# Kernel optimization log

Measured on AMD Instinct MI355X. Metric: run time of the kernel, lower is better.

Reference implementation:

```python
import jax, jax.numpy as jnp
import numpy as np

WS = (2, 6, 12)          # window_size (Z, H, W)
DIM = 192
HEADS = 6
TOW = 240                # type_of_windows = (8//2)*(360//6)
NW = 720                 # total number of windows = 3 * TOW
L = WS[0] * WS[1] * WS[2]  # 144 tokens per window


def _position_index(ws):
    """Replicates EarthAttention3D._construct_index (static int index)."""
    zi = np.arange(ws[0]); zj = -np.arange(ws[0]) * ws[0]
    hi = np.arange(ws[1]); hj = -np.arange(ws[1]) * ws[1]
    w = np.arange(ws[2])
    c1 = np.stack(np.meshgrid(zi, hi, w, indexing='ij')).reshape(3, -1)
    c2 = np.stack(np.meshgrid(zj, hj, w, indexing='ij')).reshape(3, -1)
    coords = (c1[:, :, None] - c2[:, None, :]).transpose(1, 2, 0)  # (L, L, 3)
    coords[:, :, 2] += ws[2] - 1
    coords[:, :, 1] *= 2 * ws[2] - 1
    coords[:, :, 0] *= (2 * ws[2] - 1) * ws[1] * ws[1]
    return coords.sum(-1).reshape(-1)  # (L*L,)

POS_INDEX = jnp.asarray(_position_index(WS))


def setup_inputs() -> dict:
    key = jax.random.key(0)
    ks = jax.random.split(key, 4)
    table_len = (2 * WS[2] - 1) * WS[1] * WS[1] * WS[0] * WS[0]  # 3312
    return {
        "x": jax.random.normal(ks[0], (NW, L, DIM), jnp.float32),
        "mask": jnp.zeros((NW, L, L), jnp.float32),
        "w1": jax.random.normal(ks[1], (3 * DIM, DIM), jnp.float32) * 0.02,
        "b1": jnp.zeros((3 * DIM,), jnp.float32),
        "w2": jax.random.normal(ks[2], (DIM, DIM), jnp.float32) * 0.02,
        "b2": jnp.zeros((DIM,), jnp.float32),
        "bias_table": jax.random.normal(ks[3], (table_len, TOW, HEADS), jnp.float32) * 0.02,
    }


def reference(x, mask, w1, b1, w2, b2, bias_table):
    Wn, Ltok, dim = x.shape
    hd = dim // HEADS
    scale = hd ** -0.5
    # qkv projection: (Wn, L, 3, H, hd) -> q,k,v each (Wn, H, L, hd)
    qkv = (x @ w1.T + b1).reshape(Wn, Ltok, 3, HEADS, hd)
    qkv = jnp.transpose(qkv, (2, 0, 3, 1, 4))
    q, k, v = qkv[0], qkv[1], qkv[2]
    attn = jnp.einsum('whid,whjd->whij', q * scale, k)  # (Wn, H, L, L)
    # Earth-specific bias: gather table -> (L, L, TOW, H) -> (TOW, H, L, L)
    bias = bias_table[POS_INDEX].reshape(Ltok, Ltok, TOW, HEADS)
    bias = jnp.transpose(bias, (2, 3, 0, 1))
    # tile across window axis exactly like the concat loop, then slice
    reps = Wn // TOW + 1
    bias = jnp.tile(bias, (reps, 1, 1, 1))[:Wn][None]  # (1, Wn, H, L, L)
    attn = attn[None] + bias                            # (1, Wn, H, L, L)
    attn = attn + mask[None, :, None, :, :]             # mask.unsqueeze(1).unsqueeze(0)
    attn = jax.nn.softmax(attn, axis=-1)
    out = jnp.einsum('bwhij,whjd->bwhid', attn, v)      # (1, Wn, H, L, hd)
    out = jnp.transpose(out, (0, 1, 3, 2, 4)).reshape(Wn, Ltok, dim)
    out = out @ w2.T + b2
    return out
```

## Files before the change

kernel.cpp:

```cpp
#include <hip/hip_runtime.h>
#include <cstdint>
#include <cstddef>


using short8 = __attribute__((ext_vector_type(8))) short;
using f32x4  = __attribute__((ext_vector_type(4))) float;

constexpr int kNW = 720;
constexpr float kScale = 0.17677669529663687f;
constexpr size_t kQKVElems = (size_t)kNW * 6 * 144 * 32;

__device__ __forceinline__ ushort bf16_rne(float f) {
  uint u = __builtin_bit_cast(uint, f);
  return (ushort)((u + 0x7FFFu + ((u >> 16) & 1u)) >> 16);
}
__device__ __forceinline__ float bf16_to_f(ushort h) {
  uint u = ((uint)h) << 16;
  return __builtin_bit_cast(float, u);
}
__device__ __forceinline__ uint pack_hl(float f) {
  const ushort h = bf16_rne(f);
  const ushort l = bf16_rne(f - bf16_to_f(h));
  return ((uint)h << 16) | l;
}

__global__ __launch_bounds__(256) void prep_kernel(
    const float* __restrict__ src, ushort* __restrict__ dh,
    ushort* __restrict__ dl, int n)
{
  const int i = blockIdx.x * 256 + threadIdx.x;
  if (i < n) {
    const float f = src[i];
    const ushort h = bf16_rne(f);
    dh[i] = h;
    dl[i] = bf16_rne(f - bf16_to_f(h));
  }
}

__global__ __launch_bounds__(256) void btT_kernel(
    const float* __restrict__ bt, float* __restrict__ btT)
{
  __shared__ float T[48][49];
  const int pb = (blockIdx.x % 69) * 48;
  const int bb = (blockIdx.x / 69) * 48;
  const int tid = threadIdx.x;
  for (int f = tid; f < 2304; f += 256) {
    const int r = f / 48, c = f % 48;
    T[r][c] = bt[(size_t)(pb + r) * 1440 + bb + c];
  }
  __syncthreads();
  for (int f = tid; f < 2304; f += 256) {
    const int r = f % 48, c = f / 48;
    btT[(size_t)(bb + c) * 3312 + pb + r] = T[r][c];
  }
}

template <bool IS_QKV>
__global__ __launch_bounds__(512) void gemm_kernel(
    const float* __restrict__ Xf, const uint* __restrict__ Xp,
    const ushort* __restrict__ Wh, const ushort* __restrict__ Wl,
    const float* __restrict__ bias,
    uint* __restrict__ qp, uint* __restrict__ kp, uint* __restrict__ vp,
    float* __restrict__ fout)
{
  __shared__ ushort Ah[128][40], Al[128][40];
  __shared__ ushort Bh[192][40], Bl[192][40];

  const int bid = blockIdx.x;
  const int mtile = IS_QKV ? bid / 3 : bid;
  const int col0  = IS_QKV ? (bid % 3) * 192 : 0;
  const int row0 = mtile * 128;
  const int tid = threadIdx.x;
  const int wave = tid >> 6, lane = tid & 63;
  const int rr = lane & 15, kg = lane >> 4;
  const int wm = wave >> 2, wn = wave & 3;

  f32x4 acc[4][3];
#pragma unroll
  for (int a = 0; a < 4; ++a)
#pragma unroll
    for (int b = 0; b < 3; ++b) acc[a][b] = (f32x4){0.f, 0.f, 0.f, 0.f};

  for (int kc = 0; kc < 192; kc += 32) {
#pragma unroll
    for (int u = 0; u < 2; ++u) {
      const int sl = tid + u * 512;
      const int r = sl >> 3, s = sl & 7;
      if constexpr (IS_QKV) {
        float4 xv = *(const float4*)&Xf[(size_t)(row0 + r) * 192 + kc + s * 4];
        ushort4 hv, lv;
        hv.x = bf16_rne(xv.x); lv.x = bf16_rne(xv.x - bf16_to_f(hv.x));
        hv.y = bf16_rne(xv.y); lv.y = bf16_rne(xv.y - bf16_to_f(hv.y));
        hv.z = bf16_rne(xv.z); lv.z = bf16_rne(xv.z - bf16_to_f(hv.z));
        hv.w = bf16_rne(xv.w); lv.w = bf16_rne(xv.w - bf16_to_f(hv.w));
        *(ushort4*)&Ah[r][s * 4] = hv;
        *(ushort4*)&Al[r][s * 4] = lv;
      } else {
        uint4 a = *(const uint4*)&Xp[(size_t)(row0 + r) * 192 + kc + s * 4];
        uint2 hh, ll;
        hh.x = (a.x >> 16) | (a.y & 0xffff0000u);
        hh.y = (a.z >> 16) | (a.w & 0xffff0000u);
        ll.x = (a.x & 0xffffu) | (a.y << 16);
        ll.y = (a.z & 0xffffu) | (a.w << 16);
        *(uint2*)&Ah[r][s * 4] = hh;
        *(uint2*)&Al[r][s * 4] = ll;
      }
    }
#pragma unroll
    for (int u = 0; u < 3; ++u) {
      const int idx = tid + u * 512;
      const int n = idx >> 3, s2 = idx & 7;
      const size_t g = (size_t)(col0 + n) * 192 + kc + s2 * 4;
      *(uint2*)&Bh[n][s2 * 4] = *(const uint2*)&Wh[g];
      *(uint2*)&Bl[n][s2 * 4] = *(const uint2*)&Wl[g];
    }
    __syncthreads();

    short8 ah[4], al_[4], bh[3], bl[3];
#pragma unroll
    for (int mt = 0; mt < 4; ++mt) {
      const int r = wm * 64 + mt * 16 + rr;
      ah[mt]  = *(const short8*)&Ah[r][kg * 8];
      al_[mt] = *(const short8*)&Al[r][kg * 8];
    }
#pragma unroll
    for (int nt = 0; nt < 3; ++nt) {
      const int n = wn * 48 + nt * 16 + rr;
      bh[nt] = *(const short8*)&Bh[n][kg * 8];
      bl[nt] = *(const short8*)&Bl[n][kg * 8];
    }
#pragma unroll
    for (int mt = 0; mt < 4; ++mt)
#pragma unroll
      for (int nt = 0; nt < 3; ++nt) {
        acc[mt][nt] = __builtin_amdgcn_mfma_f32_16x16x32_bf16(ah[mt],  bh[nt], acc[mt][nt], 0, 0, 0);
        acc[mt][nt] = __builtin_amdgcn_mfma_f32_16x16x32_bf16(ah[mt],  bl[nt], acc[mt][nt], 0, 0, 0);
        acc[mt][nt] = __builtin_amdgcn_mfma_f32_16x16x32_bf16(al_[mt], bh[nt], acc[mt][nt], 0, 0, 0);
      }
    __syncthreads();
  }

  if (IS_QKV) {
    const int t = col0 / 192;
    uint* dst = (t == 0) ? qp : (t == 1) ? kp : vp;
    const float sc = (t == 0) ? kScale : 1.0f;
#pragma unroll
    for (int nt = 0; nt < 3; ++nt) {
      const int c0 = wn * 48 + nt * 16;
      const int hh = c0 >> 5;
      const int d0 = (c0 & 31) + rr;
      const float bcol = bias[col0 + c0 + rr];
#pragma unroll
      for (int mt = 0; mt < 4; ++mt)
#pragma unroll
        for (int reg = 0; reg < 4; ++reg) {
          const int grow = row0 + wm * 64 + mt * 16 + kg * 4 + reg;
          const int w = grow / 144;
          const int l = grow % 144;
          dst[(((size_t)(w * 6 + hh)) * 144 + l) * 32 + d0] =
              pack_hl((acc[mt][nt][reg] + bcol) * sc);
        }
    }
  } else {
#pragma unroll
    for (int nt = 0; nt < 3; ++nt) {
      const int c = wn * 48 + nt * 16 + rr;
      const float bcol = bias[c];
#pragma unroll
      for (int mt = 0; mt < 4; ++mt)
#pragma unroll
        for (int reg = 0; reg < 4; ++reg) {
          const int grow = row0 + wm * 64 + mt * 16 + kg * 4 + reg;
          fout[(size_t)grow * 192 + c] = acc[mt][nt][reg] + bcol;
        }
    }
  }
}

__global__ __launch_bounds__(576) void attn_kernel(
    const uint* __restrict__ qp, const uint* __restrict__ kp,
    const uint* __restrict__ vp, const float* __restrict__ mask,
    const float* __restrict__ btT, uint* __restrict__ aop)
{
  __shared__ ushort Ks_[2][144][40];
  __shared__ ushort Vt[2][32][168];

  const int bid = blockIdx.x;
  const int wid = (bid & 7) * 540 + (bid >> 3);
  const int w = wid / 6, h = wid % 6;
  const int tid = threadIdx.x;
  const int wave = tid >> 6, lane = tid & 63;
  const int rr = lane & 15, kg = lane >> 4;
  const size_t base = (size_t)(w * 6 + h) * 4608;
  const float* mrow = mask + (size_t)w * 20736;
  const float* brow = btT + (size_t)((w % 240) * 6 + h) * 3312;

  const int i0 = wave * 16;
  const int i = i0 + rr;
  const int pi = 828 * (i / 72) + 23 * ((i / 12) % 6) + (i % 12) + 11;

  const uint4 qa = *(const uint4*)&qp[base + (size_t)i * 32 + kg * 8];
  const uint4 qb = *(const uint4*)&qp[base + (size_t)i * 32 + kg * 8 + 4];
  float4 mv[9], bv[9];
#pragma unroll
  for (int jt = 0; jt < 9; ++jt) {
    const int jb = jt * 16 + kg * 4;
    mv[jt] = *(const float4*)&mrow[(size_t)i * 144 + jb];
    const int pjb = 1656 * (jb / 72) + 138 * ((jb / 12) % 6) - (jb % 12);
    bv[jt] = *(const float4*)&brow[pi + pjb - 3];
  }

  for (int f = tid; f < 1152; f += 576) {
    const int l = f >> 3, d0 = (f & 7) * 4;
    const uint4 kv = *(const uint4*)&kp[base + l * 32 + d0];
    ushort4 hk, lk;
    hk.x = (ushort)(kv.x >> 16); lk.x = (ushort)(kv.x & 0xffff);
    hk.y = (ushort)(kv.y >> 16); lk.y = (ushort)(kv.y & 0xffff);
    hk.z = (ushort)(kv.z >> 16); lk.z = (ushort)(kv.z & 0xffff);
    hk.w = (ushort)(kv.w >> 16); lk.w = (ushort)(kv.w & 0xffff);
    *(ushort4*)&Ks_[0][l][d0] = hk;
    *(ushort4*)&Ks_[1][l][d0] = lk;
    const uint4 vv = *(const uint4*)&vp[base + l * 32 + d0];
    Vt[0][d0 + 0][l] = (ushort)(vv.x >> 16); Vt[1][d0 + 0][l] = (ushort)(vv.x & 0xffff);
    Vt[0][d0 + 1][l] = (ushort)(vv.y >> 16); Vt[1][d0 + 1][l] = (ushort)(vv.y & 0xffff);
    Vt[0][d0 + 2][l] = (ushort)(vv.z >> 16); Vt[1][d0 + 2][l] = (ushort)(vv.z & 0xffff);
    Vt[0][d0 + 3][l] = (ushort)(vv.w >> 16); Vt[1][d0 + 3][l] = (ushort)(vv.w & 0xffff);
  }
  if (tid < 512) {
    const int d = tid >> 4, j = 144 + (tid & 15);
    Vt[0][d][j] = 0;
    Vt[1][d][j] = 0;
  }
  __syncthreads();

  union { short8 v; uint u[4]; } QH, QL;
  QH.u[0] = (qa.x >> 16) | (qa.y & 0xffff0000u);
  QH.u[1] = (qa.z >> 16) | (qa.w & 0xffff0000u);
  QH.u[2] = (qb.x >> 16) | (qb.y & 0xffff0000u);
  QH.u[3] = (qb.z >> 16) | (qb.w & 0xffff0000u);
  QL.u[0] = (qa.x & 0xffffu) | (qa.y << 16);
  QL.u[1] = (qa.z & 0xffffu) | (qa.w << 16);
  QL.u[2] = (qb.x & 0xffffu) | (qb.y << 16);
  QL.u[3] = (qb.z & 0xffffu) | (qb.w << 16);

  f32x4 acc[9];
#pragma unroll
  for (int jt = 0; jt < 9; ++jt) {
    const short8 kah = *(const short8*)&Ks_[0][jt * 16 + rr][kg * 8];
    const short8 kal = *(const short8*)&Ks_[1][jt * 16 + rr][kg * 8];
    f32x4 c = (f32x4){0.f, 0.f, 0.f, 0.f};
    c = __builtin_amdgcn_mfma_f32_16x16x32_bf16(kah, QH.v, c, 0, 0, 0);
    c = __builtin_amdgcn_mfma_f32_16x16x32_bf16(kah, QL.v, c, 0, 0, 0);
    c = __builtin_amdgcn_mfma_f32_16x16x32_bf16(kal, QH.v, c, 0, 0, 0);
    c[0] += bv[jt].w + mv[jt].x;
    c[1] += bv[jt].z + mv[jt].y;
    c[2] += bv[jt].y + mv[jt].z;
    c[3] += bv[jt].x + mv[jt].w;
    acc[jt] = c;
  }

  float m = -1e30f;
#pragma unroll
  for (int jt = 0; jt < 9; ++jt)
    m = fmaxf(m, fmaxf(fmaxf(acc[jt][0], acc[jt][1]),
                       fmaxf(acc[jt][2], acc[jt][3])));
  m = fmaxf(m, __shfl_xor(m, 16));
  m = fmaxf(m, __shfl_xor(m, 32));
  float s = 0.f;
#pragma unroll
  for (int jt = 0; jt < 9; ++jt)
#pragma unroll
    for (int r = 0; r < 4; ++r) {
      acc[jt][r] = __expf(acc[jt][r] - m);
      s += acc[jt][r];
    }
  s += __shfl_xor(s, 16);
  s += __shfl_xor(s, 32);
  const float inv = 1.0f / s;

  uint wh_[10][2], wl_[10][2];
#pragma unroll
  for (int jt = 0; jt < 9; ++jt)
#pragma unroll
    for (int u = 0; u < 2; ++u) {
      const float p0 = acc[jt][2 * u] * inv, p1 = acc[jt][2 * u + 1] * inv;
      const ushort h0 = bf16_rne(p0), h1 = bf16_rne(p1);
      const ushort l0 = bf16_rne(p0 - bf16_to_f(h0));
      const ushort l1 = bf16_rne(p1 - bf16_to_f(h1));
      wh_[jt][u] = (uint)h0 | ((uint)h1 << 16);
      wl_[jt][u] = (uint)l0 | ((uint)l1 << 16);
    }
  wh_[9][0] = 0; wh_[9][1] = 0; wl_[9][0] = 0; wl_[9][1] = 0;

  __syncthreads();

  uint* scrw = (uint*)((ushort*)&Ks_[0][0][0] + wave * 1280);
  f32x4 oacc[2] = {(f32x4){0.f, 0.f, 0.f, 0.f}, (f32x4){0.f, 0.f, 0.f, 0.f}};
#pragma unroll
  for (int ks = 0; ks < 5; ++ks) {
    const int jtA = 2 * ks, jtB = 2 * ks + 1;
    *(uint2*)&scrw[rr * 20 + 2 * kg]           = make_uint2(wh_[jtA][0], wh_[jtA][1]);
    *(uint2*)&scrw[rr * 20 + 8 + 2 * kg]       = make_uint2(wh_[jtB][0], wh_[jtB][1]);
    *(uint2*)&scrw[320 + rr * 20 + 2 * kg]     = make_uint2(wl_[jtA][0], wl_[jtA][1]);
    *(uint2*)&scrw[320 + rr * 20 + 8 + 2 * kg] = make_uint2(wl_[jtB][0], wl_[jtB][1]);
    asm volatile("s_waitcnt lgkmcnt(0)" ::: "memory");
    const ushort* scr = (const ushort*)scrw;
    const short8 pfh = *(const short8*)&scr[rr * 40 + kg * 8];
    const short8 pfl = *(const short8*)&scr[640 + rr * 40 + kg * 8];
#pragma unroll
    for (int dt = 0; dt < 2; ++dt) {
      const short8 vfh = *(const short8*)&Vt[0][dt * 16 + rr][ks * 32 + kg * 8];
      const short8 vfl = *(const short8*)&Vt[1][dt * 16 + rr][ks * 32 + kg * 8];
      oacc[dt] = __builtin_amdgcn_mfma_f32_16x16x32_bf16(pfh, vfh, oacc[dt], 0, 0, 0);
      oacc[dt] = __builtin_amdgcn_mfma_f32_16x16x32_bf16(pfh, vfl, oacc[dt], 0, 0, 0);
      oacc[dt] = __builtin_amdgcn_mfma_f32_16x16x32_bf16(pfl, vfh, oacc[dt], 0, 0, 0);
    }
  }

#pragma unroll
  for (int dt = 0; dt < 2; ++dt)
#pragma unroll
    for (int r = 0; r < 4; ++r)
      aop[(size_t)(w * 144 + i0 + kg * 4 + r) * 192 + h * 32 + dt * 16 + rr] =
          pack_hl(oacc[dt][r]);
}

extern "C" void kernel_launch(void* const* d_in, const int* in_sizes, int n_in,
                              void* d_out, int out_size, void* d_ws, size_t ws_size,
                              hipStream_t stream)
{
  const float* x    = (const float*)d_in[0];
  const float* mask = (const float*)d_in[1];
  const float* w1   = (const float*)d_in[2];
  const float* b1   = (const float*)d_in[3];
  const float* w2   = (const float*)d_in[4];
  const float* b2   = (const float*)d_in[5];
  const float* bt   = (const float*)d_in[6];
  float* out = (float*)d_out;

  uint* qp  = (uint*)d_ws;
  uint* kp  = qp + kQKVElems;
  uint* vp  = kp + kQKVElems;
  uint* aop = vp + kQKVElems;
  ushort* w1h = (ushort*)aop;
  ushort* w1l = w1h + 110592;
  ushort* w2h = (ushort*)qp;
  ushort* w2l = w2h + 36864;
  float* btT = out;

  btT_kernel<<<69 * 30, 256, 0, stream>>>(bt, btT);
  prep_kernel<<<432, 256, 0, stream>>>(w1, w1h, w1l, 110592);
  gemm_kernel<true><<<810 * 3, 512, 0, stream>>>(
      x, nullptr, w1h, w1l, b1, qp, kp, vp, nullptr);
  attn_kernel<<<4320, 576, 0, stream>>>(qp, kp, vp, mask, btT, aop);
  prep_kernel<<<144, 256, 0, stream>>>(w2, w2h, w2l, 36864);
  gemm_kernel<false><<<810, 512, 0, stream>>>(
      nullptr, aop, w2h, w2l, b2, nullptr, nullptr, nullptr, out);
}
```

Before: 370.3 us.

## Cut attention register pressure: in-loop bias loads, lazy bf16 split, deferred normalization

```diff
diff --git a/kernel.cpp b/kernel.cpp
--- a/kernel.cpp
+++ b/kernel.cpp
@@ -22,6 +22,13 @@
   const ushort h = bf16_rne(f);
   const ushort l = bf16_rne(f - bf16_to_f(h));
   return ((uint)h << 16) | l;
+}
+__device__ __forceinline__ void split2(float a, float b, uint& hw, uint& lw) {
+  const ushort ha = bf16_rne(a), hb = bf16_rne(b);
+  const ushort la = bf16_rne(a - bf16_to_f(ha));
+  const ushort lb = bf16_rne(b - bf16_to_f(hb));
+  hw = (uint)ha | ((uint)hb << 16);
+  lw = (uint)la | ((uint)lb << 16);
 }
 
 __global__ __launch_bounds__(256) void prep_kernel(
@@ -184,6 +191,7 @@
 {
   __shared__ ushort Ks_[2][144][40];
   __shared__ ushort Vt[2][32][168];
+  __shared__ float Sinv[148];
 
   const int bid = blockIdx.x;
   const int wid = (bid & 7) * 540 + (bid >> 3);
@@ -201,14 +209,6 @@
 
   const uint4 qa = *(const uint4*)&qp[base + (size_t)i * 32 + kg * 8];
   const uint4 qb = *(const uint4*)&qp[base + (size_t)i * 32 + kg * 8 + 4];
-  float4 mv[9], bv[9];
-#pragma unroll
-  for (int jt = 0; jt < 9; ++jt) {
-    const int jb = jt * 16 + kg * 4;
-    mv[jt] = *(const float4*)&mrow[(size_t)i * 144 + jb];
-    const int pjb = 1656 * (jb / 72) + 138 * ((jb / 12) % 6) - (jb % 12);
-    bv[jt] = *(const float4*)&brow[pi + pjb - 3];
-  }
 
   for (int f = tid; f < 1152; f += 576) {
     const int l = f >> 3, d0 = (f & 7) * 4;
@@ -246,17 +246,22 @@
   f32x4 acc[9];
 #pragma unroll
   for (int jt = 0; jt < 9; ++jt) {
+    const int jb = jt * 16 + kg * 4;
+    const float4 mv = *(const float4*)&mrow[(size_t)i * 144 + jb];
+    const int pjb = 1656 * (jb / 72) + 138 * ((jb / 12) % 6) - (jb % 12);
+    const float4 bv = *(const float4*)&brow[pi + pjb - 3];
     const short8 kah = *(const short8*)&Ks_[0][jt * 16 + rr][kg * 8];
     const short8 kal = *(const short8*)&Ks_[1][jt * 16 + rr][kg * 8];
     f32x4 c = (f32x4){0.f, 0.f, 0.f, 0.f};
     c = __builtin_amdgcn_mfma_f32_16x16x32_bf16(kah, QH.v, c, 0, 0, 0);
     c = __builtin_amdgcn_mfma_f32_16x16x32_bf16(kah, QL.v, c, 0, 0, 0);
     c = __builtin_amdgcn_mfma_f32_16x16x32_bf16(kal, QH.v, c, 0, 0, 0);
-    c[0] += bv[jt].w + mv[jt].x;
-    c[1] += bv[jt].z + mv[jt].y;
-    c[2] += bv[jt].y + mv[jt].z;
-    c[3] += bv[jt].x + mv[jt].w;
+    c[0] += bv.w + mv.x;
+    c[1] += bv.z + mv.y;
+    c[2] += bv.y + mv.z;
+    c[3] += bv.x + mv.w;
     acc[jt] = c;
+    __builtin_amdgcn_sched_barrier(0x38F);
   }
 
   float m = -1e30f;
@@ -276,21 +281,7 @@
     }
   s += __shfl_xor(s, 16);
   s += __shfl_xor(s, 32);
-  const float inv = 1.0f / s;
-
-  uint wh_[10][2], wl_[10][2];
-#pragma unroll
-  for (int jt = 0; jt < 9; ++jt)
-#pragma unroll
-    for (int u = 0; u < 2; ++u) {
-      const float p0 = acc[jt][2 * u] * inv, p1 = acc[jt][2 * u + 1] * inv;
-      const ushort h0 = bf16_rne(p0), h1 = bf16_rne(p1);
-      const ushort l0 = bf16_rne(p0 - bf16_to_f(h0));
-      const ushort l1 = bf16_rne(p1 - bf16_to_f(h1));
-      wh_[jt][u] = (uint)h0 | ((uint)h1 << 16);
-      wl_[jt][u] = (uint)l0 | ((uint)l1 << 16);
-    }
-  wh_[9][0] = 0; wh_[9][1] = 0; wl_[9][0] = 0; wl_[9][1] = 0;
+  if (kg == 0) Sinv[i] = 1.0f / s;
 
   __syncthreads();
 
@@ -298,11 +289,19 @@
   f32x4 oacc[2] = {(f32x4){0.f, 0.f, 0.f, 0.f}, (f32x4){0.f, 0.f, 0.f, 0.f}};
 #pragma unroll
   for (int ks = 0; ks < 5; ++ks) {
-    const int jtA = 2 * ks, jtB = 2 * ks + 1;
-    *(uint2*)&scrw[rr * 20 + 2 * kg]           = make_uint2(wh_[jtA][0], wh_[jtA][1]);
-    *(uint2*)&scrw[rr * 20 + 8 + 2 * kg]       = make_uint2(wh_[jtB][0], wh_[jtB][1]);
-    *(uint2*)&scrw[320 + rr * 20 + 2 * kg]     = make_uint2(wl_[jtA][0], wl_[jtA][1]);
-    *(uint2*)&scrw[320 + rr * 20 + 8 + 2 * kg] = make_uint2(wl_[jtB][0], wl_[jtB][1]);
+    uint h0, h1, h2, h3, l0, l1, l2, l3;
+    split2(acc[2 * ks][0], acc[2 * ks][1], h0, l0);
+    split2(acc[2 * ks][2], acc[2 * ks][3], h1, l1);
+    if (2 * ks + 1 < 9) {
+      split2(acc[2 * ks + 1][0], acc[2 * ks + 1][1], h2, l2);
+      split2(acc[2 * ks + 1][2], acc[2 * ks + 1][3], h3, l3);
+    } else {
+      h2 = h3 = l2 = l3 = 0;
+    }
+    *(uint2*)&scrw[rr * 20 + 2 * kg]           = make_uint2(h0, h1);
+    *(uint2*)&scrw[rr * 20 + 8 + 2 * kg]       = make_uint2(h2, h3);
+    *(uint2*)&scrw[320 + rr * 20 + 2 * kg]     = make_uint2(l0, l1);
+    *(uint2*)&scrw[320 + rr * 20 + 8 + 2 * kg] = make_uint2(l2, l3);
     asm volatile("s_waitcnt lgkmcnt(0)" ::: "memory");
     const ushort* scr = (const ushort*)scrw;
     const short8 pfh = *(const short8*)&scr[rr * 40 + kg * 8];
@@ -317,12 +316,14 @@
     }
   }
 
+  const float4 sv4 = *(const float4*)&Sinv[i0 + kg * 4];
+  const float svr[4] = {sv4.x, sv4.y, sv4.z, sv4.w};
 #pragma unroll
   for (int dt = 0; dt < 2; ++dt)
 #pragma unroll
     for (int r = 0; r < 4; ++r)
       aop[(size_t)(w * 144 + i0 + kg * 4 + r) * 192 + h * 32 + dt * 16 + rr] =
-          pack_hl(oacc[dt][r]);
+          pack_hl(oacc[dt][r] * svr[r]);
 }
 
 extern "C" void kernel_launch(void* const* d_in, const int* in_sizes, int n_in,
```

New measurement: 395.1 us. +6.7%, slower.

## Load K fragments directly from global and defer V staging past QK^T

Applied to the files above, without the earlier changes.

```diff
diff --git a/kernel.cpp b/kernel.cpp
--- a/kernel.cpp
+++ b/kernel.cpp
@@ -182,8 +182,8 @@
     const uint* __restrict__ vp, const float* __restrict__ mask,
     const float* __restrict__ btT, uint* __restrict__ aop)
 {
-  __shared__ ushort Ks_[2][144][40];
   __shared__ ushort Vt[2][32][168];
+  __shared__ uint Scr[9][640];
 
   const int bid = blockIdx.x;
   const int wid = (bid & 7) * 540 + (bid >> 3);
@@ -199,6 +199,9 @@
   const int i = i0 + rr;
   const int pi = 828 * (i / 72) + 23 * ((i / 12) % 6) + (i % 12) + 11;
 
+  const uint4 rv0 = *(const uint4*)&vp[base + (size_t)tid * 4];
+  const uint4 rv1 = *(const uint4*)&vp[base + (size_t)(tid + 576) * 4];
+
   const uint4 qa = *(const uint4*)&qp[base + (size_t)i * 32 + kg * 8];
   const uint4 qb = *(const uint4*)&qp[base + (size_t)i * 32 + kg * 8 + 4];
   float4 mv[9], bv[9];
@@ -209,29 +212,6 @@
     const int pjb = 1656 * (jb / 72) + 138 * ((jb / 12) % 6) - (jb % 12);
     bv[jt] = *(const float4*)&brow[pi + pjb - 3];
   }
-
-  for (int f = tid; f < 1152; f += 576) {
-    const int l = f >> 3, d0 = (f & 7) * 4;
-    const uint4 kv = *(const uint4*)&kp[base + l * 32 + d0];
-    ushort4 hk, lk;
-    hk.x = (ushort)(kv.x >> 16); lk.x = (ushort)(kv.x & 0xffff);
-    hk.y = (ushort)(kv.y >> 16); lk.y = (ushort)(kv.y & 0xffff);
-    hk.z = (ushort)(kv.z >> 16); lk.z = (ushort)(kv.z & 0xffff);
-    hk.w = (ushort)(kv.w >> 16); lk.w = (ushort)(kv.w & 0xffff);
-    *(ushort4*)&Ks_[0][l][d0] = hk;
-    *(ushort4*)&Ks_[1][l][d0] = lk;
-    const uint4 vv = *(const uint4*)&vp[base + l * 32 + d0];
-    Vt[0][d0 + 0][l] = (ushort)(vv.x >> 16); Vt[1][d0 + 0][l] = (ushort)(vv.x & 0xffff);
-    Vt[0][d0 + 1][l] = (ushort)(vv.y >> 16); Vt[1][d0 + 1][l] = (ushort)(vv.y & 0xffff);
-    Vt[0][d0 + 2][l] = (ushort)(vv.z >> 16); Vt[1][d0 + 2][l] = (ushort)(vv.z & 0xffff);
-    Vt[0][d0 + 3][l] = (ushort)(vv.w >> 16); Vt[1][d0 + 3][l] = (ushort)(vv.w & 0xffff);
-  }
-  if (tid < 512) {
-    const int d = tid >> 4, j = 144 + (tid & 15);
-    Vt[0][d][j] = 0;
-    Vt[1][d][j] = 0;
-  }
-  __syncthreads();
 
   union { short8 v; uint u[4]; } QH, QL;
   QH.u[0] = (qa.x >> 16) | (qa.y & 0xffff0000u);
@@ -246,12 +226,22 @@
   f32x4 acc[9];
 #pragma unroll
   for (int jt = 0; jt < 9; ++jt) {
-    const short8 kah = *(const short8*)&Ks_[0][jt * 16 + rr][kg * 8];
-    const short8 kal = *(const short8*)&Ks_[1][jt * 16 + rr][kg * 8];
+    const uint* krow = &kp[base + (size_t)(jt * 16 + rr) * 32 + kg * 8];
+    const uint4 ka = *(const uint4*)&krow[0];
+    const uint4 kb = *(const uint4*)&krow[4];
+    union { short8 v; uint u[4]; } KH, KL;
+    KH.u[0] = (ka.x >> 16) | (ka.y & 0xffff0000u);
+    KH.u[1] = (ka.z >> 16) | (ka.w & 0xffff0000u);
+    KH.u[2] = (kb.x >> 16) | (kb.y & 0xffff0000u);
+    KH.u[3] = (kb.z >> 16) | (kb.w & 0xffff0000u);
+    KL.u[0] = (ka.x & 0xffffu) | (ka.y << 16);
+    KL.u[1] = (ka.z & 0xffffu) | (ka.w << 16);
+    KL.u[2] = (kb.x & 0xffffu) | (kb.y << 16);
+    KL.u[3] = (kb.z & 0xffffu) | (kb.w << 16);
     f32x4 c = (f32x4){0.f, 0.f, 0.f, 0.f};
-    c = __builtin_amdgcn_mfma_f32_16x16x32_bf16(kah, QH.v, c, 0, 0, 0);
-    c = __builtin_amdgcn_mfma_f32_16x16x32_bf16(kah, QL.v, c, 0, 0, 0);
-    c = __builtin_amdgcn_mfma_f32_16x16x32_bf16(kal, QH.v, c, 0, 0, 0);
+    c = __builtin_amdgcn_mfma_f32_16x16x32_bf16(KH.v, QH.v, c, 0, 0, 0);
+    c = __builtin_amdgcn_mfma_f32_16x16x32_bf16(KH.v, QL.v, c, 0, 0, 0);
+    c = __builtin_amdgcn_mfma_f32_16x16x32_bf16(KL.v, QH.v, c, 0, 0, 0);
     c[0] += bv[jt].w + mv[jt].x;
     c[1] += bv[jt].z + mv[jt].y;
     c[2] += bv[jt].y + mv[jt].z;
@@ -292,9 +282,27 @@
     }
   wh_[9][0] = 0; wh_[9][1] = 0; wl_[9][0] = 0; wl_[9][1] = 0;
 
+  {
+    const int l = tid >> 3, d0 = (tid & 7) * 4;
+    Vt[0][d0 + 0][l] = (ushort)(rv0.x >> 16); Vt[1][d0 + 0][l] = (ushort)(rv0.x & 0xffff);
+    Vt[0][d0 + 1][l] = (ushort)(rv0.y >> 16); Vt[1][d0 + 1][l] = (ushort)(rv0.y & 0xffff);
+    Vt[0][d0 + 2][l] = (ushort)(rv0.z >> 16); Vt[1][d0 + 2][l] = (ushort)(rv0.z & 0xffff);
+    Vt[0][d0 + 3][l] = (ushort)(rv0.w >> 16); Vt[1][d0 + 3][l] = (ushort)(rv0.w & 0xffff);
+    const int f1 = tid + 576;
+    const int l1 = f1 >> 3, d1 = (f1 & 7) * 4;
+    Vt[0][d1 + 0][l1] = (ushort)(rv1.x >> 16); Vt[1][d1 + 0][l1] = (ushort)(rv1.x & 0xffff);
+    Vt[0][d1 + 1][l1] = (ushort)(rv1.y >> 16); Vt[1][d1 + 1][l1] = (ushort)(rv1.y & 0xffff);
+    Vt[0][d1 + 2][l1] = (ushort)(rv1.z >> 16); Vt[1][d1 + 2][l1] = (ushort)(rv1.z & 0xffff);
+    Vt[0][d1 + 3][l1] = (ushort)(rv1.w >> 16); Vt[1][d1 + 3][l1] = (ushort)(rv1.w & 0xffff);
+  }
+  if (tid < 512) {
+    const int d = tid >> 4, j = 144 + (tid & 15);
+    Vt[0][d][j] = 0;
+    Vt[1][d][j] = 0;
+  }
   __syncthreads();
 
-  uint* scrw = (uint*)((ushort*)&Ks_[0][0][0] + wave * 1280);
+  uint* scrw = Scr[wave];
   f32x4 oacc[2] = {(f32x4){0.f, 0.f, 0.f, 0.f}, (f32x4){0.f, 0.f, 0.f, 0.f}};
 #pragma unroll
   for (int ks = 0; ks < 5; ++ks) {
```

Result: slower. 405.8 us (+9.6%).

## Process two heads per attention block with double-buffered K/V prefetch

Applied to the files above, without the earlier changes.

```diff
diff --git a/kernel.cpp b/kernel.cpp
--- a/kernel.cpp
+++ b/kernel.cpp
@@ -177,30 +177,20 @@
   }
 }
 
-__global__ __launch_bounds__(576) void attn_kernel(
-    const uint* __restrict__ qp, const uint* __restrict__ kp,
-    const uint* __restrict__ vp, const float* __restrict__ mask,
-    const float* __restrict__ btT, uint* __restrict__ aop)
-{
-  __shared__ ushort Ks_[2][144][40];
-  __shared__ ushort Vt[2][32][168];
-
-  const int bid = blockIdx.x;
-  const int wid = (bid & 7) * 540 + (bid >> 3);
-  const int w = wid / 6, h = wid % 6;
-  const int tid = threadIdx.x;
-  const int wave = tid >> 6, lane = tid & 63;
-  const int rr = lane & 15, kg = lane >> 4;
-  const size_t base = (size_t)(w * 6 + h) * 4608;
-  const float* mrow = mask + (size_t)w * 20736;
-  const float* brow = btT + (size_t)((w % 240) * 6 + h) * 3312;
-
+__device__ __forceinline__ void attn_unit(
+    const ushort (&KsH)[144][40], const ushort (&KsL)[144][40],
+    const ushort (&VtH)[32][168], const ushort (&VtL)[32][168],
+    uint* __restrict__ scrw,
+    const uint* __restrict__ qpb, const float* __restrict__ mrow,
+    const float* __restrict__ brow, uint* __restrict__ aopb,
+    int wave, int rr, int kg)
+{
   const int i0 = wave * 16;
   const int i = i0 + rr;
   const int pi = 828 * (i / 72) + 23 * ((i / 12) % 6) + (i % 12) + 11;
 
-  const uint4 qa = *(const uint4*)&qp[base + (size_t)i * 32 + kg * 8];
-  const uint4 qb = *(const uint4*)&qp[base + (size_t)i * 32 + kg * 8 + 4];
+  const uint4 qa = *(const uint4*)&qpb[(size_t)i * 32 + kg * 8];
+  const uint4 qb = *(const uint4*)&qpb[(size_t)i * 32 + kg * 8 + 4];
   float4 mv[9], bv[9];
 #pragma unroll
   for (int jt = 0; jt < 9; ++jt) {
@@ -209,29 +199,6 @@
     const int pjb = 1656 * (jb / 72) + 138 * ((jb / 12) % 6) - (jb % 12);
     bv[jt] = *(const float4*)&brow[pi + pjb - 3];
   }
-
-  for (int f = tid; f < 1152; f += 576) {
-    const int l = f >> 3, d0 = (f & 7) * 4;
-    const uint4 kv = *(const uint4*)&kp[base + l * 32 + d0];
-    ushort4 hk, lk;
-    hk.x = (ushort)(kv.x >> 16); lk.x = (ushort)(kv.x & 0xffff);
-    hk.y = (ushort)(kv.y >> 16); lk.y = (ushort)(kv.y & 0xffff);
-    hk.z = (ushort)(kv.z >> 16); lk.z = (ushort)(kv.z & 0xffff);
-    hk.w = (ushort)(kv.w >> 16); lk.w = (ushort)(kv.w & 0xffff);
-    *(ushort4*)&Ks_[0][l][d0] = hk;
-    *(ushort4*)&Ks_[1][l][d0] = lk;
-    const uint4 vv = *(const uint4*)&vp[base + l * 32 + d0];
-    Vt[0][d0 + 0][l] = (ushort)(vv.x >> 16); Vt[1][d0 + 0][l] = (ushort)(vv.x & 0xffff);
-    Vt[0][d0 + 1][l] = (ushort)(vv.y >> 16); Vt[1][d0 + 1][l] = (ushort)(vv.y & 0xffff);
-    Vt[0][d0 + 2][l] = (ushort)(vv.z >> 16); Vt[1][d0 + 2][l] = (ushort)(vv.z & 0xffff);
-    Vt[0][d0 + 3][l] = (ushort)(vv.w >> 16); Vt[1][d0 + 3][l] = (ushort)(vv.w & 0xffff);
-  }
-  if (tid < 512) {
-    const int d = tid >> 4, j = 144 + (tid & 15);
-    Vt[0][d][j] = 0;
-    Vt[1][d][j] = 0;
-  }
-  __syncthreads();
 
   union { short8 v; uint u[4]; } QH, QL;
   QH.u[0] = (qa.x >> 16) | (qa.y & 0xffff0000u);
@@ -246,8 +213,8 @@
   f32x4 acc[9];
 #pragma unroll
   for (int jt = 0; jt < 9; ++jt) {
-    const short8 kah = *(const short8*)&Ks_[0][jt * 16 + rr][kg * 8];
-    const short8 kal = *(const short8*)&Ks_[1][jt * 16 + rr][kg * 8];
+    const short8 kah = *(const short8*)&KsH[jt * 16 + rr][kg * 8];
+    const short8 kal = *(const short8*)&KsL[jt * 16 + rr][kg * 8];
     f32x4 c = (f32x4){0.f, 0.f, 0.f, 0.f};
     c = __builtin_amdgcn_mfma_f32_16x16x32_bf16(kah, QH.v, c, 0, 0, 0);
     c = __builtin_amdgcn_mfma_f32_16x16x32_bf16(kah, QL.v, c, 0, 0, 0);
@@ -292,9 +259,6 @@
     }
   wh_[9][0] = 0; wh_[9][1] = 0; wl_[9][0] = 0; wl_[9][1] = 0;
 
-  __syncthreads();
-
-  uint* scrw = (uint*)((ushort*)&Ks_[0][0][0] + wave * 1280);
   f32x4 oacc[2] = {(f32x4){0.f, 0.f, 0.f, 0.f}, (f32x4){0.f, 0.f, 0.f, 0.f}};
 #pragma unroll
   for (int ks = 0; ks < 5; ++ks) {
@@ -309,20 +273,120 @@
     const short8 pfl = *(const short8*)&scr[640 + rr * 40 + kg * 8];
 #pragma unroll
     for (int dt = 0; dt < 2; ++dt) {
-      const short8 vfh = *(const short8*)&Vt[0][dt * 16 + rr][ks * 32 + kg * 8];
-      const short8 vfl = *(const short8*)&Vt[1][dt * 16 + rr][ks * 32 + kg * 8];
+      const short8 vfh = *(const short8*)&VtH[dt * 16 + rr][ks * 32 + kg * 8];
+      const short8 vfl = *(const short8*)&VtL[dt * 16 + rr][ks * 32 + kg * 8];
       oacc[dt] = __builtin_amdgcn_mfma_f32_16x16x32_bf16(pfh, vfh, oacc[dt], 0, 0, 0);
       oacc[dt] = __builtin_amdgcn_mfma_f32_16x16x32_bf16(pfh, vfl, oacc[dt], 0, 0, 0);
       oacc[dt] = __builtin_amdgcn_mfma_f32_16x16x32_bf16(pfl, vfh, oacc[dt], 0, 0, 0);
     }
+    asm volatile("s_waitcnt lgkmcnt(0)" ::: "memory");
   }
 
 #pragma unroll
   for (int dt = 0; dt < 2; ++dt)
 #pragma unroll
     for (int r = 0; r < 4; ++r)
-      aop[(size_t)(w * 144 + i0 + kg * 4 + r) * 192 + h * 32 + dt * 16 + rr] =
+      aopb[(size_t)(i0 + kg * 4 + r) * 192 + dt * 16 + rr] =
           pack_hl(oacc[dt][r]);
+}
+
+__global__ __launch_bounds__(576) void attn_kernel(
+    const uint* __restrict__ qp, const uint* __restrict__ kp,
+    const uint* __restrict__ vp, const float* __restrict__ mask,
+    const float* __restrict__ btT, uint* __restrict__ aop)
+{
+  __shared__ __align__(16) ushort Ks_[2][2][144][40];
+  __shared__ __align__(16) ushort Vt[2][2][32][168];
+  __shared__ __align__(16) uint Scr[9][640];
+
+  const int tid = threadIdx.x;
+  const int wave = tid >> 6, lane = tid & 63;
+  const int rr = lane & 15, kg = lane >> 4;
+
+  const int b = blockIdx.x;
+  const int q = (b & 7) * 270 + (b >> 3);
+  const int w = q / 3;
+  const int h0 = (q % 3) * 2;
+  const size_t base0 = (size_t)(w * 6 + h0) * 4608;
+  const size_t base1 = base0 + 4608;
+  const float* mrow = mask + (size_t)w * 20736;
+  const float* brow0 = btT + (size_t)((w % 240) * 6 + h0) * 3312;
+  const float* brow1 = brow0 + 3312;
+  uint* aopb0 = aop + (size_t)w * 144 * 192 + h0 * 32;
+  uint* aopb1 = aopb0 + 32;
+
+  const int l0 = tid >> 3, d0 = (tid & 7) * 4;
+  const int f1 = tid + 576;
+  const int l1 = f1 >> 3, d1 = (f1 & 7) * 4;
+  {
+    const uint4 kvA = *(const uint4*)&kp[base0 + l0 * 32 + d0];
+    const uint4 vvA = *(const uint4*)&vp[base0 + l0 * 32 + d0];
+    const uint4 kvB = *(const uint4*)&kp[base0 + l1 * 32 + d1];
+    const uint4 vvB = *(const uint4*)&vp[base0 + l1 * 32 + d1];
+    ushort4 hk, lk;
+    hk.x = (ushort)(kvA.x >> 16); lk.x = (ushort)(kvA.x & 0xffff);
+    hk.y = (ushort)(kvA.y >> 16); lk.y = (ushort)(kvA.y & 0xffff);
+    hk.z = (ushort)(kvA.z >> 16); lk.z = (ushort)(kvA.z & 0xffff);
+    hk.w = (ushort)(kvA.w >> 16); lk.w = (ushort)(kvA.w & 0xffff);
+    *(ushort4*)&Ks_[0][0][l0][d0] = hk;
+    *(ushort4*)&Ks_[0][1][l0][d0] = lk;
+    hk.x = (ushort)(kvB.x >> 16); lk.x = (ushort)(kvB.x & 0xffff);
+    hk.y = (ushort)(kvB.y >> 16); lk.y = (ushort)(kvB.y & 0xffff);
+    hk.z = (ushort)(kvB.z >> 16); lk.z = (ushort)(kvB.z & 0xffff);
+    hk.w = (ushort)(kvB.w >> 16); lk.w = (ushort)(kvB.w & 0xffff);
+    *(ushort4*)&Ks_[0][0][l1][d1] = hk;
+    *(ushort4*)&Ks_[0][1][l1][d1] = lk;
+    Vt[0][0][d0 + 0][l0] = (ushort)(vvA.x >> 16); Vt[0][1][d0 + 0][l0] = (ushort)(vvA.x & 0xffff);
+    Vt[0][0][d0 + 1][l0] = (ushort)(vvA.y >> 16); Vt[0][1][d0 + 1][l0] = (ushort)(vvA.y & 0xffff);
+    Vt[0][0][d0 + 2][l0] = (ushort)(vvA.z >> 16); Vt[0][1][d0 + 2][l0] = (ushort)(vvA.z & 0xffff);
+    Vt[0][0][d0 + 3][l0] = (ushort)(vvA.w >> 16); Vt[0][1][d0 + 3][l0] = (ushort)(vvA.w & 0xffff);
+    Vt[0][0][d1 + 0][l1] = (ushort)(vvB.x >> 16); Vt[0][1][d1 + 0][l1] = (ushort)(vvB.x & 0xffff);
+    Vt[0][0][d1 + 1][l1] = (ushort)(vvB.y >> 16); Vt[0][1][d1 + 1][l1] = (ushort)(vvB.y & 0xffff);
+    Vt[0][0][d1 + 2][l1] = (ushort)(vvB.z >> 16); Vt[0][1][d1 + 2][l1] = (ushort)(vvB.z & 0xffff);
+    Vt[0][0][d1 + 3][l1] = (ushort)(vvB.w >> 16); Vt[0][1][d1 + 3][l1] = (ushort)(vvB.w & 0xffff);
+  }
+  for (int f = tid; f < 2048; f += 576) {
+    const int bu = f >> 10, pl = (f >> 9) & 1, d = (f >> 4) & 31, j = 144 + (f & 15);
+    Vt[bu][pl][d][j] = 0;
+  }
+
+  const uint4 kv1A = *(const uint4*)&kp[base1 + l0 * 32 + d0];
+  const uint4 vv1A = *(const uint4*)&vp[base1 + l0 * 32 + d0];
+  const uint4 kv1B = *(const uint4*)&kp[base1 + l1 * 32 + d1];
+  const uint4 vv1B = *(const uint4*)&vp[base1 + l1 * 32 + d1];
+
+  __syncthreads();
+
+  attn_unit(Ks_[0][0], Ks_[0][1], Vt[0][0], Vt[0][1], Scr[wave],
+            qp + base0, mrow, brow0, aopb0, wave, rr, kg);
+
+  {
+    ushort4 hk, lk;
+    hk.x = (ushort)(kv1A.x >> 16); lk.x = (ushort)(kv1A.x & 0xffff);
+    hk.y = (ushort)(kv1A.y >> 16); lk.y = (ushort)(kv1A.y & 0xffff);
+    hk.z = (ushort)(kv1A.z >> 16); lk.z = (ushort)(kv1A.z & 0xffff);
+    hk.w = (ushort)(kv1A.w >> 16); lk.w = (ushort)(kv1A.w & 0xffff);
+    *(ushort4*)&Ks_[1][0][l0][d0] = hk;
+    *(ushort4*)&Ks_[1][1][l0][d0] = lk;
+    hk.x = (ushort)(kv1B.x >> 16); lk.x = (ushort)(kv1B.x & 0xffff);
+    hk.y = (ushort)(kv1B.y >> 16); lk.y = (ushort)(kv1B.y & 0xffff);
+    hk.z = (ushort)(kv1B.z >> 16); lk.z = (ushort)(kv1B.z & 0xffff);
+    hk.w = (ushort)(kv1B.w >> 16); lk.w = (ushort)(kv1B.w & 0xffff);
+    *(ushort4*)&Ks_[1][0][l1][d1] = hk;
+    *(ushort4*)&Ks_[1][1][l1][d1] = lk;
+    Vt[1][0][d0 + 0][l0] = (ushort)(vv1A.x >> 16); Vt[1][1][d0 + 0][l0] = (ushort)(vv1A.x & 0xffff);
+    Vt[1][0][d0 + 1][l0] = (ushort)(vv1A.y >> 16); Vt[1][1][d0 + 1][l0] = (ushort)(vv1A.y & 0xffff);
+    Vt[1][0][d0 + 2][l0] = (ushort)(vv1A.z >> 16); Vt[1][1][d0 + 2][l0] = (ushort)(vv1A.z & 0xffff);
+    Vt[1][0][d0 + 3][l0] = (ushort)(vv1A.w >> 16); Vt[1][1][d0 + 3][l0] = (ushort)(vv1A.w & 0xffff);
+    Vt[1][0][d1 + 0][l1] = (ushort)(vv1B.x >> 16); Vt[1][1][d1 + 0][l1] = (ushort)(vv1B.x & 0xffff);
+    Vt[1][0][d1 + 1][l1] = (ushort)(vv1B.y >> 16); Vt[1][1][d1 + 1][l1] = (ushort)(vv1B.y & 0xffff);
+    Vt[1][0][d1 + 2][l1] = (ushort)(vv1B.z >> 16); Vt[1][1][d1 + 2][l1] = (ushort)(vv1B.z & 0xffff);
+    Vt[1][0][d1 + 3][l1] = (ushort)(vv1B.w >> 16); Vt[1][1][d1 + 3][l1] = (ushort)(vv1B.w & 0xffff);
+  }
+  __syncthreads();
+
+  attn_unit(Ks_[1][0], Ks_[1][1], Vt[1][0], Vt[1][1], Scr[wave],
+            qp + base1, mrow, brow1, aopb1, wave, rr, kg);
 }
 
 extern "C" void kernel_launch(void* const* d_in, const int* in_sizes, int n_in,
@@ -352,7 +416,7 @@
   prep_kernel<<<432, 256, 0, stream>>>(w1, w1h, w1l, 110592);
   gemm_kernel<true><<<810 * 3, 512, 0, stream>>>(
       x, nullptr, w1h, w1l, b1, qp, kp, vp, nullptr);
-  attn_kernel<<<4320, 576, 0, stream>>>(qp, kp, vp, mask, btT, aop);
+  attn_kernel<<<2160, 576, 0, stream>>>(qp, kp, vp, mask, btT, aop);
   prep_kernel<<<144, 256, 0, stream>>>(w2, w2h, w2l, 36864);
   gemm_kernel<false><<<810, 512, 0, stream>>>(
       nullptr, aop, w2h, w2l, b2, nullptr, nullptr, nullptr, out);
```

After: 363.4 us. No clear change (-1.9%).
